# Performance work log

Measured on AMD Instinct MI355X. Metric: run time of the kernel, lower is better.

Reference implementation:

```python
import jax, jax.numpy as jnp
import numpy as np
from jax import lax

DK, K = 3, 3          # duration_kernel_size, kernel_size
PD, P = 1, 1          # duration_padding, padding
RANKS = 3


def setup_inputs() -> dict:
    key = jax.random.key(0)
    k1, k2, k3, k4, k5 = jax.random.split(key, 5)
    B, Cin, Cout, D, H, W = 2, 64, 64, 8, 128, 128
    x = jax.random.normal(k1, (B, Cin, D, H, W), dtype=jnp.float32)
    # 1x1x1 conv weights (squeezed to [out, in])
    head_w = jax.random.normal(k2, (Cout, Cin), dtype=jnp.float32) * 0.1
    tail_w = jax.random.normal(k3, (Cout, Cout), dtype=jnp.float32) * 0.1
    std = float(np.sqrt(2.0 / RANKS))
    U_w = jax.random.normal(k4, (DK * K * K, RANKS), dtype=jnp.float32) * std
    V_w = jax.random.normal(k5, (Cout, RANKS), dtype=jnp.float32) * std
    return {"x": x, "head_w": head_w, "tail_w": tail_w, "U_w": U_w, "V_w": V_w}


def _forward(x, head_w, tail_w, U_w, V_w):
    B, Cin, D, H, W = x.shape
    Cout = head_w.shape[0]
    R = U_w.shape[1]
    # head 1x1x1 conv
    h = jnp.einsum('bidhw,oi->bodhw', x, head_w)
    # replicate pad (torch F.pad mode='replicate' == jnp.pad mode='edge')
    hp = jnp.pad(h, ((0, 0), (0, 0), (PD, PD), (P, P), (P, P)), mode='edge')
    # einsum('bcdhwk,kr->bcdhwr') over unfolded windows == depthwise conv with
    # a kernel shared across channels: fold (B,C) into the batch dim and run a
    # 1->R channel 3D correlation (avoids materializing the [.,27] unfold tensor).
    xin = hp.reshape(B * Cout, 1, D + 2 * PD, H + 2 * P, W + 2 * P)
    kern = U_w.T.reshape(R, 1, DK, K, K)  # unfold flattens as (dk, kh, kw)
    Up = lax.conv_general_dilated(
        xin, kern, window_strides=(1, 1, 1), padding='VALID',
        dimension_numbers=('NCDHW', 'OIDHW', 'NCDHW'))
    Up = Up.reshape(B, Cout, R, D, H, W)
    # _l2norm over rank dim: u / (1e-6 + ||u||_2)
    norm = jnp.sqrt(jnp.sum(Up * Up, axis=2, keepdims=True))
    Un = Up / (1e-6 + norm)
    # V projection: einsum('bcdhwk,cr->brdhwk') with k==1
    Vp = jnp.einsum('bcdhw,cr->brdhw', h, V_w)
    # UV: einsum('bcdhwr,brdhwk->bcdhwk') with k==1 -> contract over r
    UV = jnp.einsum('bcrdhw,brdhw->bcdhw', Un, Vp)
    # tail 1x1x1 conv
    out = jnp.einsum('bcdhw,oc->bodhw', UV, tail_w)
    return out


def reference(x, head_w, tail_w, U_w, V_w):
    return _forward(x, head_w, tail_w, U_w, V_w)
```

## Files before the change

### kernel.cpp

```cpp
#include <hip/hip_runtime.h>

#define Bn   2
#define Cn   64
#define Dd   8
#define Hd   128
#define Wd   128
#define HW   16384
#define DHW  131072
#define NPOS 262144
#define NELEM 16777216

typedef __attribute__((ext_vector_type(8))) short short8;
typedef __attribute__((ext_vector_type(4))) float floatx4;

__device__ __forceinline__ short f2bf(float f) {
    union { float f; unsigned u; } v; v.f = f;
    unsigned r = (v.u + 0x7FFFu + ((v.u >> 16) & 1u)) >> 16;
    return (short)r;
}
__device__ __forceinline__ float bf2f(short s) {
    union { unsigned u; float f; } v; v.u = ((unsigned)(unsigned short)s) << 16;
    return v.f;
}
__device__ __forceinline__ void split2(float f, short& hi, short& lo) {
    union { float f; unsigned u; } a; a.f = f;
    unsigned hu = a.u & 0xFFFF0000u;
    hi = (short)(hu >> 16);
    union { unsigned u; float f; } hb; hb.u = hu;
    union { float f; unsigned u; } lb; lb.f = f - hb.f;
    lo = (short)(lb.u >> 16);
}

__global__ __launch_bounds__(256) void k_prep(const float* __restrict__ head_w,
                                              const float* __restrict__ tail_w,
                                              const float* __restrict__ V_w,
                                              short* __restrict__ Whh, short* __restrict__ Whl,
                                              short* __restrict__ Wth, short* __restrict__ Wtl)
{
    int t = threadIdx.x;
#pragma unroll
    for (int rep = 0; rep < 16; ++rep) {
        int idx = rep * 256 + t;
        short hh, hl;
        split2(head_w[idx], hh, hl);
        Whh[idx] = hh; Whl[idx] = hl;
        split2(tail_w[idx], hh, hl);
        Wth[idx] = hh; Wtl[idx] = hl;
    }
    if (t < 192) {
        int r = t >> 6, i = t & 63;
        float s = 0.f;
        for (int cc = 0; cc < 64; ++cc) s += V_w[cc * 3 + r] * head_w[cc * 64 + i];
        short hh, hl;
        split2(s, hh, hl);
        Whh[(64 + r) * 64 + i] = hh;
        Whl[(64 + r) * 64 + i] = hl;
    }
#pragma unroll
    for (int rep = 0; rep < 4; ++rep) {
        int idx = rep * 256 + t;
        if (idx < 832) { Whh[67 * 64 + idx] = 0; Whl[67 * 64 + idx] = 0; }
    }
}

__global__ __launch_bounds__(256) void k_headm(const float* __restrict__ x,
                                               const short* __restrict__ Whh,
                                               const short* __restrict__ Whl,
                                               float* __restrict__ h,
                                               float* __restrict__ Vp)
{
    __shared__ __align__(16) char smem[52 * 1024];
    short* Xh = (short*)smem;
    short* Xl = (short*)(smem + 16 * 1024);
    short* Bh = (short*)(smem + 32 * 1024);
    short* Bl = (short*)(smem + 42 * 1024);
    float* Cb = (float*)smem;

    int t  = threadIdx.x;
    int p0 = blockIdx.x * 128;
    int b  = p0 >> 17;
    int s0 = p0 & (DHW - 1);
    const float* xb = x + ((size_t)b * Cn) * DHW + s0;

    int pp = t & 127;
    int ho = t >> 7;
#pragma unroll
    for (int pass = 0; pass < 4; ++pass) {
        int in0 = pass * 16 + ho * 8;
        short8 vh, vl;
#pragma unroll
        for (int j = 0; j < 8; ++j) {
            short hh, hl;
            split2(xb[(size_t)(in0 + j) * DHW + pp], hh, hl);
            vh[j] = hh; vl[j] = hl;
        }
        int blk  = ((in0 >> 5) << 3) | (pp >> 4);
        int slot = (((in0 >> 3) & 3) << 4) | (pp & 15);
        *(short8*)&Xh[(blk * 64 + slot) * 8] = vh;
        *(short8*)&Xl[(blk * 64 + slot) * 8] = vl;
    }
#pragma unroll
    for (int pass = 0; pass < 3; ++pass) {
        int unit = pass * 256 + t;
        if (unit < 640) {
            int o   = unit - (unit / 80) * 80;
            int oc  = unit / 80;
            int in0 = oc * 8;
            int blk  = ((o >> 4) << 1) | (in0 >> 5);
            int slot = (((in0 >> 3) & 3) << 4) | (o & 15);
            *(short8*)&Bh[(blk * 64 + slot) * 8] = *(const short8*)&Whh[o * 64 + in0];
            *(short8*)&Bl[(blk * 64 + slot) * 8] = *(const short8*)&Whl[o * 64 + in0];
        }
    }
    __syncthreads();

    int lane = t & 63;
    int w    = t >> 6;
    floatx4 acc[2][5];
#pragma unroll
    for (int mt = 0; mt < 2; ++mt)
#pragma unroll
        for (int nt = 0; nt < 5; ++nt) acc[mt][nt] = (floatx4)0.f;

    const short8* XhV = (const short8*)Xh;
    const short8* XlV = (const short8*)Xl;
    const short8* BhV = (const short8*)Bh;
    const short8* BlV = (const short8*)Bl;
#pragma unroll
    for (int ks = 0; ks < 2; ++ks) {
        short8 ah0 = XhV[(ks * 8 + w * 2 + 0) * 64 + lane];
        short8 ah1 = XhV[(ks * 8 + w * 2 + 1) * 64 + lane];
        short8 al0 = XlV[(ks * 8 + w * 2 + 0) * 64 + lane];
        short8 al1 = XlV[(ks * 8 + w * 2 + 1) * 64 + lane];
#pragma unroll
        for (int nt = 0; nt < 5; ++nt) {
            short8 bh = BhV[(nt * 2 + ks) * 64 + lane];
            short8 bl = BlV[(nt * 2 + ks) * 64 + lane];
            acc[0][nt] = __builtin_amdgcn_mfma_f32_16x16x32_bf16(al0, bl, acc[0][nt], 0, 0, 0);
            acc[0][nt] = __builtin_amdgcn_mfma_f32_16x16x32_bf16(al0, bh, acc[0][nt], 0, 0, 0);
            acc[0][nt] = __builtin_amdgcn_mfma_f32_16x16x32_bf16(ah0, bl, acc[0][nt], 0, 0, 0);
            acc[0][nt] = __builtin_amdgcn_mfma_f32_16x16x32_bf16(ah0, bh, acc[0][nt], 0, 0, 0);
            acc[1][nt] = __builtin_amdgcn_mfma_f32_16x16x32_bf16(al1, bl, acc[1][nt], 0, 0, 0);
            acc[1][nt] = __builtin_amdgcn_mfma_f32_16x16x32_bf16(al1, bh, acc[1][nt], 0, 0, 0);
            acc[1][nt] = __builtin_amdgcn_mfma_f32_16x16x32_bf16(ah1, bl, acc[1][nt], 0, 0, 0);
            acc[1][nt] = __builtin_amdgcn_mfma_f32_16x16x32_bf16(ah1, bh, acc[1][nt], 0, 0, 0);
        }
    }

    __syncthreads();
    int outc = lane & 15;
    int quad = lane >> 4;
#pragma unroll
    for (int mt = 0; mt < 2; ++mt)
#pragma unroll
        for (int nt = 0; nt < 5; ++nt) {
            int o   = nt * 16 + outc;
            int pos = w * 32 + mt * 16 + quad * 4;
            *(floatx4*)&Cb[o * 132 + pos] = acc[mt][nt];
        }
    __syncthreads();

    int xr = (t & 31) * 4;
    int ob = t >> 5;
#pragma unroll
    for (int pass = 0; pass < 9; ++pass) {
        int o = pass * 8 + ob;
        floatx4 vv = *(const floatx4*)&Cb[o * 132 + xr];
        if (o < 64) {
            *(floatx4*)&h[((size_t)(b * Cn + o)) * DHW + s0 + xr] = vv;
        } else if (o < 67) {
            *(floatx4*)&Vp[((size_t)(b * 3 + (o - 64))) * DHW + s0 + xr] = vv;
        }
    }
}

__global__ __launch_bounds__(256) void k_uv(const float* __restrict__ h,
                                            const float* __restrict__ Vp,
                                            const float* __restrict__ U_w,
                                            float* __restrict__ UV)
{
    __shared__ float tile[Dd][10][Wd];

    int blk = blockIdx.x;
    int yt  = blk & 15;
    int bc  = blk >> 4;
    int b   = bc >> 6;
    int y0  = yt * 8;
    int t   = threadIdx.x;

    const float* hb = h + (size_t)bc * DHW;
#pragma unroll
    for (int rep = 0; rep < 10; ++rep) {
        int idx = rep * 256 + t;
        int d   = idx / 320;
        int rem = idx - d * 320;
        int lr  = rem >> 5;
        int x4  = (rem & 31) * 4;
        int zy  = y0 - 1 + lr;
        zy = zy < 0 ? 0 : (zy > Hd - 1 ? Hd - 1 : zy);
        *(floatx4*)&tile[d][lr][x4] = *(const floatx4*)(hb + d * HW + zy * Wd + x4);
    }
    __syncthreads();

    int xl = t & 31;
    int yr = t >> 5;
    int xq = xl * 4;
    int y  = y0 + yr;
    int xmi = (xl == 0)  ? 0   : xq - 1;
    int xpi = (xl == 31) ? 127 : xq + 4;

    float a0[8][4], a1[8][4], a2[8][4];
#pragma unroll
    for (int d = 0; d < 8; ++d)
#pragma unroll
        for (int j = 0; j < 4; ++j) { a0[d][j] = 0.f; a1[d][j] = 0.f; a2[d][j] = 0.f; }

#define CONTRIB(dd, dk)                                                   \
    {                                                                     \
        _Pragma("unroll")                                                 \
        for (int kh = 0; kh < 3; ++kh) {                                  \
            _Pragma("unroll")                                             \
            for (int kw = 0; kw < 3; ++kw) {                              \
                const int kk = (((dk) * 3 + kh) * 3 + kw) * 3;            \
                const float u0 = U_w[kk + 0];                             \
                const float u1 = U_w[kk + 1];                             \
                const float u2 = U_w[kk + 2];                             \
                _Pragma("unroll")                                         \
                for (int j = 0; j < 4; ++j) {                             \
                    a0[dd][j] += wv[kh][kw + j] * u0;                     \
                    a1[dd][j] += wv[kh][kw + j] * u1;                     \
                    a2[dd][j] += wv[kh][kw + j] * u2;                     \
                }                                                         \
            }                                                             \
        }                                                                 \
    }

#pragma unroll
    for (int sl = 0; sl < 8; ++sl) {
        float wv[3][6];
#pragma unroll
        for (int kh = 0; kh < 3; ++kh) {
            const float* row = &tile[sl][yr + kh][0];
            floatx4 c = *(const floatx4*)&row[xq];
            wv[kh][0] = row[xmi];
            wv[kh][1] = c[0]; wv[kh][2] = c[1];
            wv[kh][3] = c[2]; wv[kh][4] = c[3];
            wv[kh][5] = row[xpi];
        }
        CONTRIB(sl, 1);
        if (sl == 0) CONTRIB(0, 0);
        if (sl < 7)  CONTRIB(sl + 1, 0);
        if (sl > 0)  CONTRIB(sl - 1, 2);
        if (sl == 7) CONTRIB(7, 2);
    }
#undef CONTRIB

    const float* vpb = Vp + (size_t)b * 3 * DHW + y * Wd + xq;
    float* uvb       = UV + (size_t)bc * DHW + y * Wd + xq;
#pragma unroll
    for (int d = 0; d < 8; ++d) {
        floatx4 v0 = *(const floatx4*)(vpb + (size_t)d * HW);
        floatx4 v1 = *(const floatx4*)(vpb + (size_t)DHW + d * HW);
        floatx4 v2 = *(const floatx4*)(vpb + (size_t)2 * DHW + d * HW);
        floatx4 ov;
#pragma unroll
        for (int j = 0; j < 4; ++j) {
            float nrm = sqrtf(a0[d][j] * a0[d][j] + a1[d][j] * a1[d][j] + a2[d][j] * a2[d][j]);
            float inv = 1.f / (1e-6f + nrm);
            ov[j] = (a0[d][j] * v0[j] + a1[d][j] * v1[j] + a2[d][j] * v2[j]) * inv;
        }
        *(floatx4*)(uvb + (size_t)d * HW) = ov;
    }
}

__global__ __launch_bounds__(256) void k_tailm(const float* __restrict__ UV,
                                               const short* __restrict__ Wth,
                                               const short* __restrict__ Wtl,
                                               float* __restrict__ out)
{
    __shared__ __align__(16) char smem[48 * 1024];
    short* Xh = (short*)smem;
    short* Xl = (short*)(smem + 16 * 1024);
    short* Bh = (short*)(smem + 32 * 1024);
    short* Bl = (short*)(smem + 40 * 1024);
    float* Cb = (float*)smem;

    int t  = threadIdx.x;
    int p0 = blockIdx.x * 128;
    int b  = p0 >> 17;
    int s0 = p0 & (DHW - 1);
    const float* ub = UV + ((size_t)b * Cn) * DHW + s0;

    int pp = t & 127;
    int ho = t >> 7;
#pragma unroll
    for (int pass = 0; pass < 4; ++pass) {
        int in0 = pass * 16 + ho * 8;
        short8 vh, vl;
#pragma unroll
        for (int j = 0; j < 8; ++j) {
            short hh, hl;
            split2(ub[(size_t)(in0 + j) * DHW + pp], hh, hl);
            vh[j] = hh; vl[j] = hl;
        }
        int blk  = ((in0 >> 5) << 3) | (pp >> 4);
        int slot = (((in0 >> 3) & 3) << 4) | (pp & 15);
        *(short8*)&Xh[(blk * 64 + slot) * 8] = vh;
        *(short8*)&Xl[(blk * 64 + slot) * 8] = vl;
    }
#pragma unroll
    for (int pass = 0; pass < 2; ++pass) {
        int unit = pass * 256 + t;
        int o    = unit & 63;
        int oc   = unit >> 6;
        int in0  = oc * 8;
        int blk  = ((o >> 4) << 1) | (in0 >> 5);
        int slot = (((in0 >> 3) & 3) << 4) | (o & 15);
        *(short8*)&Bh[(blk * 64 + slot) * 8] = *(const short8*)&Wth[o * 64 + in0];
        *(short8*)&Bl[(blk * 64 + slot) * 8] = *(const short8*)&Wtl[o * 64 + in0];
    }
    __syncthreads();

    int lane = t & 63;
    int w    = t >> 6;
    floatx4 acc[2][4];
#pragma unroll
    for (int mt = 0; mt < 2; ++mt)
#pragma unroll
        for (int nt = 0; nt < 4; ++nt) acc[mt][nt] = (floatx4)0.f;

    const short8* XhV = (const short8*)Xh;
    const short8* XlV = (const short8*)Xl;
    const short8* BhV = (const short8*)Bh;
    const short8* BlV = (const short8*)Bl;
#pragma unroll
    for (int ks = 0; ks < 2; ++ks) {
        short8 ah0 = XhV[(ks * 8 + w * 2 + 0) * 64 + lane];
        short8 ah1 = XhV[(ks * 8 + w * 2 + 1) * 64 + lane];
        short8 al0 = XlV[(ks * 8 + w * 2 + 0) * 64 + lane];
        short8 al1 = XlV[(ks * 8 + w * 2 + 1) * 64 + lane];
#pragma unroll
        for (int nt = 0; nt < 4; ++nt) {
            short8 bh = BhV[(nt * 2 + ks) * 64 + lane];
            short8 bl = BlV[(nt * 2 + ks) * 64 + lane];
            acc[0][nt] = __builtin_amdgcn_mfma_f32_16x16x32_bf16(al0, bl, acc[0][nt], 0, 0, 0);
            acc[0][nt] = __builtin_amdgcn_mfma_f32_16x16x32_bf16(al0, bh, acc[0][nt], 0, 0, 0);
            acc[0][nt] = __builtin_amdgcn_mfma_f32_16x16x32_bf16(ah0, bl, acc[0][nt], 0, 0, 0);
            acc[0][nt] = __builtin_amdgcn_mfma_f32_16x16x32_bf16(ah0, bh, acc[0][nt], 0, 0, 0);
            acc[1][nt] = __builtin_amdgcn_mfma_f32_16x16x32_bf16(al1, bl, acc[1][nt], 0, 0, 0);
            acc[1][nt] = __builtin_amdgcn_mfma_f32_16x16x32_bf16(al1, bh, acc[1][nt], 0, 0, 0);
            acc[1][nt] = __builtin_amdgcn_mfma_f32_16x16x32_bf16(ah1, bl, acc[1][nt], 0, 0, 0);
            acc[1][nt] = __builtin_amdgcn_mfma_f32_16x16x32_bf16(ah1, bh, acc[1][nt], 0, 0, 0);
        }
    }

    __syncthreads();
    int outc = lane & 15;
    int quad = lane >> 4;
#pragma unroll
    for (int mt = 0; mt < 2; ++mt)
#pragma unroll
        for (int nt = 0; nt < 4; ++nt) {
            int o   = nt * 16 + outc;
            int pos = w * 32 + mt * 16 + quad * 4;
            *(floatx4*)&Cb[o * 132 + pos] = acc[mt][nt];
        }
    __syncthreads();

    int xr = (t & 31) * 4;
    int ob = t >> 5;
#pragma unroll
    for (int pass = 0; pass < 8; ++pass) {
        int o = pass * 8 + ob;
        floatx4 vv = *(const floatx4*)&Cb[o * 132 + xr];
        *(floatx4*)&out[((size_t)(b * Cn + o)) * DHW + s0 + xr] = vv;
    }
}

extern "C" void kernel_launch(void* const* d_in, const int* in_sizes, int n_in,
                              void* d_out, int out_size, void* d_ws, size_t ws_size,
                              hipStream_t stream)
{
    const float* x      = (const float*)d_in[0];
    const float* head_w = (const float*)d_in[1];
    const float* tail_w = (const float*)d_in[2];
    const float* U_w    = (const float*)d_in[3];
    const float* V_w    = (const float*)d_in[4];
    float* out = (float*)d_out;

    float* h   = (float*)d_ws;
    float* Vp  = h + (size_t)NELEM;
    float* UVf = Vp + (size_t)Bn * 3 * DHW;
    short* Whh = (short*)(UVf + (size_t)NELEM);
    short* Whl = Whh + 80 * 64;
    short* Wth = Whl + 80 * 64;
    short* Wtl = Wth + 64 * 64;

    k_prep<<<1, 256, 0, stream>>>(head_w, tail_w, V_w, Whh, Whl, Wth, Wtl);
    k_headm<<<NPOS / 128, 256, 0, stream>>>(x, Whh, Whl, h, Vp);
    k_uv<<<Bn * Cn * (Hd / 8), 256, 0, stream>>>(h, Vp, U_w, UVf);
    k_tailm<<<NPOS / 128, 256, 0, stream>>>(UVf, Wth, Wtl, out);
}
```

Measured before the change: 244.9 us.

## Split the UV depth loop into two templated halves and fetch halo columns by lane shuffle

The depthwise-conv/UV kernel now computes its 8 depth slices as two templated passes of 4 slices each. This halves the live accumulator arrays from 96 to 48 floats per thread, which should lower VGPR pressure and raise occupancy. Each pass re-reads one extra boundary slice (two extra slice passes in total), a small cost. The left and right halo columns now come from neighbouring lanes through __shfl_up/__shfl_down instead of extra scalar LDS reads, with edge replication handled by lane-index checks.

```diff
diff --git a/kernel.cpp b/kernel.cpp
--- a/kernel.cpp
+++ b/kernel.cpp
@@ -174,44 +174,18 @@
     }
 }
 
-__global__ __launch_bounds__(256) void k_uv(const float* __restrict__ h,
-                                            const float* __restrict__ Vp,
-                                            const float* __restrict__ U_w,
-                                            float* __restrict__ UV)
-{
-    __shared__ float tile[Dd][10][Wd];
-
-    int blk = blockIdx.x;
-    int yt  = blk & 15;
-    int bc  = blk >> 4;
-    int b   = bc >> 6;
-    int y0  = yt * 8;
-    int t   = threadIdx.x;
-
-    const float* hb = h + (size_t)bc * DHW;
-#pragma unroll
-    for (int rep = 0; rep < 10; ++rep) {
-        int idx = rep * 256 + t;
-        int d   = idx / 320;
-        int rem = idx - d * 320;
-        int lr  = rem >> 5;
-        int x4  = (rem & 31) * 4;
-        int zy  = y0 - 1 + lr;
-        zy = zy < 0 ? 0 : (zy > Hd - 1 ? Hd - 1 : zy);
-        *(floatx4*)&tile[d][lr][x4] = *(const floatx4*)(hb + d * HW + zy * Wd + x4);
-    }
-    __syncthreads();
-
-    int xl = t & 31;
-    int yr = t >> 5;
-    int xq = xl * 4;
-    int y  = y0 + yr;
-    int xmi = (xl == 0)  ? 0   : xq - 1;
-    int xpi = (xl == 31) ? 127 : xq + 4;
-
-    float a0[8][4], a1[8][4], a2[8][4];
-#pragma unroll
-    for (int d = 0; d < 8; ++d)
+template<int D0>
+__device__ __forceinline__ void uv_half(const float (*tile)[10][Wd], int yr, int xq, int xl,
+                                        const float* __restrict__ U_w,
+                                        const float* __restrict__ vpb,
+                                        float* __restrict__ uvb)
+{
+    constexpr int SL0 = (D0 == 0) ? 0 : 3;
+    constexpr int SL1 = (D0 == 0) ? 4 : 7;
+
+    float a0[4][4], a1[4][4], a2[4][4];
+#pragma unroll
+    for (int d = 0; d < 4; ++d)
 #pragma unroll
         for (int j = 0; j < 4; ++j) { a0[d][j] = 0.f; a1[d][j] = 0.f; a2[d][j] = 0.f; }
 
@@ -236,32 +210,31 @@
     }
 
 #pragma unroll
-    for (int sl = 0; sl < 8; ++sl) {
+    for (int sl = SL0; sl <= SL1; ++sl) {
         float wv[3][6];
 #pragma unroll
         for (int kh = 0; kh < 3; ++kh) {
-            const float* row = &tile[sl][yr + kh][0];
-            floatx4 c = *(const floatx4*)&row[xq];
-            wv[kh][0] = row[xmi];
-            wv[kh][1] = c[0]; wv[kh][2] = c[1];
-            wv[kh][3] = c[2]; wv[kh][4] = c[3];
-            wv[kh][5] = row[xpi];
-        }
-        CONTRIB(sl, 1);
-        if (sl == 0) CONTRIB(0, 0);
-        if (sl < 7)  CONTRIB(sl + 1, 0);
-        if (sl > 0)  CONTRIB(sl - 1, 2);
-        if (sl == 7) CONTRIB(7, 2);
+            floatx4 c = *(const floatx4*)&tile[sl][yr + kh][xq];
+            float lf = __shfl_up(c[3], 1u);
+            float rt = __shfl_down(c[0], 1u);
+            wv[kh][0] = (xl == 0)  ? c[0] : lf;
+            wv[kh][1] = c[0]; wv[kh][2] = c[1]; wv[kh][3] = c[2]; wv[kh][4] = c[3];
+            wv[kh][5] = (xl == 31) ? c[3] : rt;
+        }
+        if (sl >= D0 && sl <= D0 + 3)                   CONTRIB(sl - D0, 1);
+        if (sl + 1 >= D0 && sl + 1 <= D0 + 3)           CONTRIB(sl + 1 - D0, 0);
+        if (sl - 1 >= D0 && sl - 1 <= D0 + 3 && sl > 0) CONTRIB(sl - 1 - D0, 2);
+        if (D0 == 0 && sl == 0)                         CONTRIB(0, 0);
+        if (D0 == 4 && sl == 7)                         CONTRIB(3, 2);
     }
 #undef CONTRIB
 
-    const float* vpb = Vp + (size_t)b * 3 * DHW + y * Wd + xq;
-    float* uvb       = UV + (size_t)bc * DHW + y * Wd + xq;
-#pragma unroll
-    for (int d = 0; d < 8; ++d) {
-        floatx4 v0 = *(const floatx4*)(vpb + (size_t)d * HW);
-        floatx4 v1 = *(const floatx4*)(vpb + (size_t)DHW + d * HW);
-        floatx4 v2 = *(const floatx4*)(vpb + (size_t)2 * DHW + d * HW);
+#pragma unroll
+    for (int d = 0; d < 4; ++d) {
+        const int dg = D0 + d;
+        floatx4 v0 = *(const floatx4*)(vpb + (size_t)dg * HW);
+        floatx4 v1 = *(const floatx4*)(vpb + (size_t)DHW + (size_t)dg * HW);
+        floatx4 v2 = *(const floatx4*)(vpb + (size_t)2 * DHW + (size_t)dg * HW);
         floatx4 ov;
 #pragma unroll
         for (int j = 0; j < 4; ++j) {
@@ -269,8 +242,48 @@
             float inv = 1.f / (1e-6f + nrm);
             ov[j] = (a0[d][j] * v0[j] + a1[d][j] * v1[j] + a2[d][j] * v2[j]) * inv;
         }
-        *(floatx4*)(uvb + (size_t)d * HW) = ov;
-    }
+        *(floatx4*)(uvb + (size_t)dg * HW) = ov;
+    }
+}
+
+__global__ __launch_bounds__(256) void k_uv(const float* __restrict__ h,
+                                            const float* __restrict__ Vp,
+                                            const float* __restrict__ U_w,
+                                            float* __restrict__ UV)
+{
+    __shared__ float tile[Dd][10][Wd];
+
+    int blk = blockIdx.x;
+    int yt  = blk & 15;
+    int bc  = blk >> 4;
+    int b   = bc >> 6;
+    int y0  = yt * 8;
+    int t   = threadIdx.x;
+
+    const float* hb = h + (size_t)bc * DHW;
+#pragma unroll
+    for (int rep = 0; rep < 10; ++rep) {
+        int idx = rep * 256 + t;
+        int d   = idx / 320;
+        int rem = idx - d * 320;
+        int lr  = rem >> 5;
+        int x4  = (rem & 31) * 4;
+        int zy  = y0 - 1 + lr;
+        zy = zy < 0 ? 0 : (zy > Hd - 1 ? Hd - 1 : zy);
+        *(floatx4*)&tile[d][lr][x4] = *(const floatx4*)(hb + d * HW + zy * Wd + x4);
+    }
+    __syncthreads();
+
+    int xl = t & 31;
+    int yr = t >> 5;
+    int xq = xl * 4;
+    int y  = y0 + yr;
+
+    const float* vpb = Vp + (size_t)b * 3 * DHW + y * Wd + xq;
+    float* uvb       = UV + (size_t)bc * DHW + y * Wd + xq;
+
+    uv_half<0>(tile, yr, xq, xl, U_w, vpb, uvb);
+    uv_half<4>(tile, yr, xq, xl, U_w, vpb, uvb);
 }
 
 __global__ __launch_bounds__(256) void k_tailm(const float* __restrict__ UV,
```

Result: slower. 258.7 us (+5.6%).
